# Performance work log

Measured on AMD Instinct MI355X. Metric: run time of the kernel, lower is better.

## Reference

```python
import jax, jax.numpy as jnp
import numpy as np

EPS = 1e-6
NUM_HEADS = 8


def layer_norm(x, g, b):
    m = jnp.mean(x, axis=-1, keepdims=True)
    v = jnp.mean(jnp.square(x - m), axis=-1, keepdims=True)
    return (x - m) * jax.lax.rsqrt(v + EPS) * g + b


def dwconv3x3(x, w, b):
    # x: [B, C, H, W], w: [C, 1, 3, 3] depthwise, b: [C]
    y = jax.lax.conv_general_dilated(
        x, w, window_strides=(1, 1), padding='SAME',
        feature_group_count=x.shape[1],
        dimension_numbers=('NCHW', 'OIHW', 'NCHW'))
    return y + b[None, :, None, None]


def setup_inputs() -> dict:
    key = jax.random.key(0)
    ks = jax.random.split(key, 16)
    B, H, W, C = 4, 128, 128, 256
    N = H * W
    hid = 3 * C  # mlp_ratio=3
    s = 0.02
    return {
        'x': jax.random.normal(ks[0], (B, N, C), jnp.float32),
        'H': H,
        'W': W,
        'ln1_g': jnp.ones((C,), jnp.float32),
        'ln1_b': jnp.zeros((C,), jnp.float32),
        'qkv_w': jax.random.normal(ks[1], (C, 3 * C), jnp.float32) * s,
        'qkv_b': jnp.zeros((3 * C,), jnp.float32),
        'crpe_w': jax.random.normal(ks[2], (C, 1, 3, 3), jnp.float32) * s,
        'crpe_b': jnp.zeros((C,), jnp.float32),
        'proj_w': jax.random.normal(ks[3], (C, C), jnp.float32) * s,
        'proj_b': jnp.zeros((C,), jnp.float32),
        'ln2_g': jnp.ones((C,), jnp.float32),
        'ln2_b': jnp.zeros((C,), jnp.float32),
        'fc1_w': jax.random.normal(ks[4], (C, hid), jnp.float32) * s,
        'fc1_b': jnp.zeros((hid,), jnp.float32),
        'dconv_w': jax.random.normal(ks[5], (hid, 1, 3, 3), jnp.float32) * s,
        'dconv_b': jnp.zeros((hid,), jnp.float32),
        'fc2_w': jax.random.normal(ks[6], (hid, C), jnp.float32) * s,
        'fc2_b': jnp.zeros((C,), jnp.float32),
    }


def reference(x, H, W, ln1_g, ln1_b, qkv_w, qkv_b, crpe_w, crpe_b,
              proj_w, proj_b, ln2_g, ln2_b, fc1_w, fc1_b,
              dconv_w, dconv_b, fc2_w, fc2_b):
    B, N, C = x.shape
    h = NUM_HEADS
    d = C // h
    scale = d ** -0.5

    # --- attention branch ---
    cur = layer_norm(x, ln1_g, ln1_b)
    qkv = (cur @ qkv_w + qkv_b).reshape(B, N, 3, h, d).transpose(2, 0, 3, 1, 4)
    q, k, v = qkv[0], qkv[1], qkv[2]          # each [B, h, N, d]
    k_sm = jax.nn.softmax(k, axis=2)          # softmax over tokens N
    kv = jnp.einsum('bhnk,bhnv->bhkv', k_sm, v)      # [B, h, d, d]
    factor = jnp.einsum('bhnk,bhkv->bhnv', q, kv)    # [B, h, N, d]
    # CRPE: q * depthwise_conv(v) on the HxW grid (head-major channel layout)
    v_img = v.transpose(0, 1, 3, 2).reshape(B, C, H, W)
    conv_v = dwconv3x3(v_img, crpe_w, crpe_b).reshape(B, h, d, N).transpose(0, 1, 3, 2)
    att = scale * factor + q * conv_v         # [B, h, N, d]
    att = att.transpose(0, 2, 1, 3).reshape(B, N, C)
    x = x + (att @ proj_w + proj_b)

    # --- conv-MLP branch ---
    cur = layer_norm(x, ln2_g, ln2_b)
    hdn = cur @ fc1_w + fc1_b                 # [B, N, 3C]
    hdn_img = hdn.transpose(0, 2, 1).reshape(B, hdn.shape[-1], H, W)
    dc = dwconv3x3(hdn_img, dconv_w, dconv_b).reshape(B, hdn.shape[-1], N).transpose(0, 2, 1)
    hdn = jax.nn.gelu(hdn + dc, approximate=False)
    return x + (hdn @ fc2_w + fc2_b)
```

## Files before the change

### kernel.cpp

```cpp
#include <hip/hip_runtime.h>
#include <math.h>

#define BB   4
#define HH   128
#define WW2  128
#define NN   (HH*WW2)
#define CC   256
#define NH   8
#define HID  768
#define EPSF 1e-6f
#define SCALE 0.17677669529663687f

typedef __attribute__((ext_vector_type(8))) short s8v;
typedef __attribute__((ext_vector_type(4))) float f4v;

__device__ __forceinline__ float bf2f(ushort h) {
    union { unsigned u; float f; } x; x.u = ((unsigned)h) << 16; return x.f;
}
__device__ __forceinline__ ushort f2bf(float f) {
    union { float f; unsigned u; } x; x.f = f;
    unsigned r = (x.u + 0x7FFFu + ((x.u >> 16) & 1u)) >> 16;
    return (ushort)r;
}

typedef __attribute__((address_space(1))) unsigned gu32;
typedef __attribute__((address_space(3))) unsigned lu32;
__device__ __forceinline__ void gl_lds16(const void* g, void* l) {
    __builtin_amdgcn_global_load_lds((gu32*)g, (lu32*)l, 16, 0, 0);
}

__global__ __launch_bounds__(256) void ln_bf16v(const float* __restrict__ in,
                                                const float* __restrict__ g,
                                                const float* __restrict__ bta,
                                                ushort* __restrict__ out) {
    int row  = blockIdx.x*4 + (threadIdx.x >> 6);
    int lane = threadIdx.x & 63;
    const float* p = in + (size_t)row*CC + lane*4;
    float4 v = *(const float4*)p;
    float s  = v.x + v.y + v.z + v.w;
    float s2 = v.x*v.x + v.y*v.y + v.z*v.z + v.w*v.w;
    #pragma unroll
    for (int off = 32; off >= 1; off >>= 1) {
        s  += __shfl_xor(s, off);
        s2 += __shfl_xor(s2, off);
    }
    float mean = s * (1.0f/CC);
    float var  = s2 * (1.0f/CC) - mean*mean;
    float r    = rsqrtf(var + EPSF);
    float4 gv = *(const float4*)&g[lane*4];
    float4 bv = *(const float4*)&bta[lane*4];
    ushort4 o;
    o.x = f2bf((v.x-mean)*r*gv.x + bv.x);
    o.y = f2bf((v.y-mean)*r*gv.y + bv.y);
    o.z = f2bf((v.z-mean)*r*gv.z + bv.z);
    o.w = f2bf((v.w-mean)*r*gv.w + bv.w);
    *(ushort4*)&out[(size_t)row*CC + lane*4] = o;
}

__global__ __launch_bounds__(256) void wtrans(const float* __restrict__ w,
                                              ushort* __restrict__ wt, int K, int N) {
    __shared__ float tile[32][33];
    int k0 = blockIdx.x*32, n0 = blockIdx.y*32;
    int c = threadIdx.x & 31, r8 = threadIdx.x >> 5;
    #pragma unroll
    for (int r = 0; r < 4; ++r) {
        int kk = r8 + r*8;
        tile[kk][c] = w[(size_t)(k0+kk)*N + n0 + c];
    }
    __syncthreads();
    #pragma unroll
    for (int r = 0; r < 4; ++r) {
        int nn = r8 + r*8;
        wt[(size_t)(n0+nn)*K + k0 + c] = f2bf(tile[c][nn]);
    }
}

__global__ __launch_bounds__(256) void wtrans_proj(const float* __restrict__ w,
                                                   ushort* __restrict__ Bcat) {
    __shared__ float tile[32][33];
    int k0 = blockIdx.x*32, n0 = blockIdx.y*32;
    int c = threadIdx.x & 31, r8 = threadIdx.x >> 5;
    #pragma unroll
    for (int r = 0; r < 4; ++r) {
        int kk = r8 + r*8;
        tile[kk][c] = w[(size_t)(k0+kk)*CC + n0 + c];
    }
    __syncthreads();
    #pragma unroll
    for (int r = 0; r < 4; ++r) {
        int nn = r8 + r*8;
        ushort val = f2bf(tile[c][nn]);
        #pragma unroll
        for (int b = 0; b < BB; ++b)
            Bcat[((size_t)(b*256 + n0+nn))*512 + 256 + k0 + c] = val;
    }
}

template<int KDIM, int MODE>
__global__ __launch_bounds__(256) void mfma_gemm(const ushort* __restrict__ A,
                                                 const ushort* __restrict__ Bt,
                                                 const float* __restrict__ bias,
                                                 const float* __restrict__ resid,
                                                 void* __restrict__ Cout,
                                                 ushort* __restrict__ kbuf,
                                                 ushort* __restrict__ vbuf,
                                                 int NDIM) {
    __shared__ ushort lsA[128*32];
    __shared__ ushort lsB[128*32];
    int tid  = threadIdx.x;
    int lane = tid & 63;
    int w    = tid >> 6;
    int wm   = w >> 1, wn = w & 1;
    size_t mBase = (size_t)blockIdx.y * 128;
    int    nBase = blockIdx.x * 128;
    int lrow = lane & 15, lq = lane >> 4;

    const ushort* gA = A  + (mBase + w*32 + (lane>>2))*(size_t)KDIM + (lane&3)*8;
    const ushort* gB = Bt + ((size_t)(nBase + w*32 + (lane>>2)))*(size_t)KDIM + (lane&3)*8;
    ushort* lA = lsA + w*1024;
    ushort* lB = lsB + w*1024;

    f4v acc[4][4] = {};

    for (int k0 = 0; k0 < KDIM; k0 += 32) {
        gl_lds16(gA + k0,           lA);
        gl_lds16(gA + k0 + 16*KDIM, lA + 512);
        gl_lds16(gB + k0,           lB);
        gl_lds16(gB + k0 + 16*KDIM, lB + 512);
        __syncthreads();
        s8v af[4], bf[4];
        #pragma unroll
        for (int i = 0; i < 4; ++i)
            af[i] = *(const s8v*)&lsA[(wm*64 + i*16 + lrow)*32 + lq*8];
        #pragma unroll
        for (int j = 0; j < 4; ++j)
            bf[j] = *(const s8v*)&lsB[(wn*64 + j*16 + lrow)*32 + lq*8];
        #pragma unroll
        for (int i = 0; i < 4; ++i)
            #pragma unroll
            for (int j = 0; j < 4; ++j)
                acc[i][j] = __builtin_amdgcn_mfma_f32_16x16x32_bf16(af[i], bf[j], acc[i][j], 0, 0, 0);
        __syncthreads();
    }

    int colBase = nBase + wn*64;
    #pragma unroll
    for (int j = 0; j < 4; ++j) {
        int col = colBase + j*16 + lrow;
        float bs = bias[col];
        #pragma unroll
        for (int i = 0; i < 4; ++i) {
            #pragma unroll
            for (int r = 0; r < 4; ++r) {
                size_t row = mBase + wm*64 + i*16 + lq*4 + r;
                float v = acc[i][j][r] + bs;
                if constexpr (MODE == 0) {
                    ((ushort*)Cout)[row*(size_t)NDIM + col] = f2bf(v);
                } else if constexpr (MODE == 1) {
                    size_t idx = row*(size_t)NDIM + col;
                    ((float*)Cout)[idx] = v + resid[idx];
                } else {
                    if (col < 256)      ((ushort*)Cout)[row*512 + col] = f2bf(v);
                    else if (col < 512) kbuf[row*256 + col - 256] = f2bf(v);
                    else                vbuf[row*256 + col - 512] = f2bf(v);
                }
            }
        }
    }
}

__global__ __launch_bounds__(256) void mfma_gemm_attn(const ushort* __restrict__ aq,
                                                      const ushort* __restrict__ Bcat,
                                                      const float* __restrict__ bias,
                                                      const float* __restrict__ resid,
                                                      float* __restrict__ Cout) {
    __shared__ ushort lsA[128*32];
    __shared__ ushort lsB[128*32];
    int tid  = threadIdx.x;
    int lane = tid & 63;
    int w    = tid >> 6;
    int wm   = w >> 1, wn = w & 1;
    int b = blockIdx.z;
    size_t mBase = (size_t)b*NN + (size_t)blockIdx.y * 128;
    int    nBase = blockIdx.x * 128;
    int lrow = lane & 15, lq = lane >> 4;

    const ushort* gA = aq + (mBase + w*32 + (lane>>2))*512 + (lane&3)*8;
    const ushort* gB = Bcat + ((size_t)(b*256 + nBase + w*32 + (lane>>2)))*512 + (lane&3)*8;
    ushort* lA = lsA + w*1024;
    ushort* lB = lsB + w*1024;

    f4v acc[4][4] = {};

    for (int k0 = 0; k0 < 512; k0 += 32) {
        gl_lds16(gA + k0,          lA);
        gl_lds16(gA + k0 + 16*512, lA + 512);
        gl_lds16(gB + k0,          lB);
        gl_lds16(gB + k0 + 16*512, lB + 512);
        __syncthreads();
        s8v af[4], bf[4];
        #pragma unroll
        for (int i = 0; i < 4; ++i)
            af[i] = *(const s8v*)&lsA[(wm*64 + i*16 + lrow)*32 + lq*8];
        #pragma unroll
        for (int j = 0; j < 4; ++j)
            bf[j] = *(const s8v*)&lsB[(wn*64 + j*16 + lrow)*32 + lq*8];
        #pragma unroll
        for (int i = 0; i < 4; ++i)
            #pragma unroll
            for (int j = 0; j < 4; ++j)
                acc[i][j] = __builtin_amdgcn_mfma_f32_16x16x32_bf16(af[i], bf[j], acc[i][j], 0, 0, 0);
        __syncthreads();
    }

    int colBase = nBase + wn*64;
    #pragma unroll
    for (int j = 0; j < 4; ++j) {
        int col = colBase + j*16 + lrow;
        float bs = bias[col];
        #pragma unroll
        for (int i = 0; i < 4; ++i) {
            #pragma unroll
            for (int r = 0; r < 4; ++r) {
                size_t row = mBase + wm*64 + i*16 + lq*4 + r;
                size_t idx = row*(size_t)CC + col;
                Cout[idx] = acc[i][j][r] + bs + resid[idx];
            }
        }
    }
}

__global__ void zero_kernel(float* __restrict__ p, int nElems) {
    int i = blockIdx.x*256 + threadIdx.x;
    if (i < nElems) p[i] = 0.f;
}

__global__ __launch_bounds__(256) void kv_accum(const ushort* __restrict__ kbuf,
                                                const ushort* __restrict__ vbuf,
                                                float* __restrict__ kv_raw,
                                                float* __restrict__ ksum) {
    int blk = blockIdx.x;
    int chunk = blk & 15;
    int bh = blk >> 4;
    int b = bh >> 3, hh = bh & 7;
    int tid = threadIdx.x;
    __shared__ float ke[32][36];
    __shared__ float vv[32][36];
    int tok = tid >> 3;
    int c4  = (tid & 7) * 4;
    int kd  = tid >> 3;
    int v0  = (tid & 7) * 4;
    float acc0=0.f, acc1=0.f, acc2=0.f, acc3=0.f, ks=0.f;
    for (int it = 0; it < 32; ++it) {
        int nb = chunk*1024 + it*32;
        size_t rowoff = ((size_t)b*NN + nb + tok)*256 + hh*32 + c4;
        ushort4 k4 = *(const ushort4*)&kbuf[rowoff];
        ushort4 v4 = *(const ushort4*)&vbuf[rowoff];
        float4 kf, vf;
        kf.x = expf(bf2f(k4.x)); kf.y = expf(bf2f(k4.y));
        kf.z = expf(bf2f(k4.z)); kf.w = expf(bf2f(k4.w));
        vf.x = bf2f(v4.x); vf.y = bf2f(v4.y); vf.z = bf2f(v4.z); vf.w = bf2f(v4.w);
        *(float4*)&ke[tok][c4] = kf;
        *(float4*)&vv[tok][c4] = vf;
        __syncthreads();
        #pragma unroll
        for (int tt = 0; tt < 32; ++tt) {
            float kval = ke[tt][kd];
            float4 vr = *(const float4*)&vv[tt][v0];
            ks   += kval;
            acc0 += kval*vr.x;
            acc1 += kval*vr.y;
            acc2 += kval*vr.z;
            acc3 += kval*vr.w;
        }
        __syncthreads();
    }
    float* dst = kv_raw + ((size_t)bh*32 + kd)*32 + v0;
    atomicAdd(dst+0, acc0); atomicAdd(dst+1, acc1);
    atomicAdd(dst+2, acc2); atomicAdd(dst+3, acc3);
    if (v0 == 0) atomicAdd(&ksum[bh*32 + kd], ks);
}

__global__ __launch_bounds__(256) void kv_fold(const float* __restrict__ kv_raw,
                                               const float* __restrict__ ksum,
                                               const float* __restrict__ proj_w,
                                               ushort* __restrict__ Bcat) {
    int bh = blockIdx.x;
    int b = bh >> 3, hh = bh & 7;
    int tid = threadIdx.x;
    __shared__ float kvn[32][33];
    __shared__ float pw[32][256];
    {
        int kd = tid >> 3, v4 = (tid & 7) * 4;
        float inv = 1.0f / ksum[bh*32 + kd];
        const float* src = kv_raw + ((size_t)bh*32 + kd)*32 + v4;
        kvn[kd][v4+0] = src[0]*inv; kvn[kd][v4+1] = src[1]*inv;
        kvn[kd][v4+2] = src[2]*inv; kvn[kd][v4+3] = src[3]*inv;
    }
    for (int vd = 0; vd < 32; ++vd)
        pw[vd][tid] = proj_w[(size_t)(hh*32 + vd)*CC + tid];
    __syncthreads();
    ushort* dst = Bcat + ((size_t)(b*256 + tid))*512 + hh*32;
    for (int kd = 0; kd < 32; ++kd) {
        float acc = 0.f;
        #pragma unroll
        for (int vd = 0; vd < 32; ++vd) acc += kvn[kd][vd] * pw[vd][tid];
        dst[kd] = f2bf(SCALE * acc);
    }
}

__global__ __launch_bounds__(256) void attn_gate(const ushort* __restrict__ vbuf,
                                                 const float* __restrict__ w,
                                                 const float* __restrict__ wb,
                                                 ushort* __restrict__ aq) {
    int xq = blockIdx.x, yq = blockIdx.y, b = blockIdx.z;
    int c = threadIdx.x;
    int y0 = yq*2;

    const float* wc = w + c*9;
    float w00=wc[0], w01=wc[1], w02=wc[2],
          w10=wc[3], w11=wc[4], w12=wc[5],
          w20=wc[6], w21=wc[7], w22=wc[8];
    float bw = wb[c];

    const ushort* vbase = vbuf + (size_t)b*NN*256 + c;
    auto ldv = [&](int yy, int xx) -> float {
        if ((unsigned)yy >= (unsigned)HH || (unsigned)xx >= (unsigned)WW2) return 0.f;
        return bf2f(vbase[((size_t)yy*WW2 + xx)*256]);
    };

    int x0 = xq*32;
    float rp[4], rc[4];
    #pragma unroll
    for (int r = 0; r < 4; ++r) {
        rp[r] = ldv(y0-1+r, x0-1);
        rc[r] = ldv(y0-1+r, x0);
    }

    #pragma unroll 4
    for (int i = 0; i < 32; ++i) {
        int x = x0 + i;
        float rn[4];
        #pragma unroll
        for (int r = 0; r < 4; ++r) rn[r] = ldv(y0-1+r, x+1);
        #pragma unroll
        for (int o = 0; o < 2; ++o) {
            float conv = bw + w00*rp[o] + w01*rc[o] + w02*rn[o]
                            + w10*rp[o+1] + w11*rc[o+1] + w12*rn[o+1]
                            + w20*rp[o+2] + w21*rc[o+2] + w22*rn[o+2];
            size_t bn = (size_t)b*NN + (size_t)(y0+o)*WW2 + x;
            float qc = bf2f(aq[bn*512 + c]);
            aq[bn*512 + 256 + c] = f2bf(qc*conv);
        }
        #pragma unroll
        for (int r = 0; r < 4; ++r) { rp[r] = rc[r]; rc[r] = rn[r]; }
    }
}

__global__ __launch_bounds__(384) void dconv_gelu_row2(const ushort* __restrict__ hdn,
                                                       const float* __restrict__ w,
                                                       const float* __restrict__ bias,
                                                       ushort* __restrict__ out) {
    int xq = blockIdx.x, yq = blockIdx.y, bz = blockIdx.z;
    int c = threadIdx.x * 2;
    int y0 = yq*2;

    float wA[9], wB[9];
    #pragma unroll
    for (int i = 0; i < 9; ++i) { wA[i] = w[c*9 + i]; wB[i] = w[(c+1)*9 + i]; }
    float bw0 = bias[c], bw1 = bias[c+1];

    const ushort* base = hdn + (size_t)bz*NN*HID + c;
    auto ld2 = [&](int yy, int xx) -> float2 {
        if ((unsigned)yy >= (unsigned)HH || (unsigned)xx >= (unsigned)WW2)
            return make_float2(0.f, 0.f);
        ushort2 u = *(const ushort2*)&base[((size_t)yy*WW2 + xx)*HID];
        return make_float2(bf2f(u.x), bf2f(u.y));
    };

    int x0 = xq*32;
    float2 rp[4], rc[4];
    #pragma unroll
    for (int r = 0; r < 4; ++r) {
        rp[r] = ld2(y0-1+r, x0-1);
        rc[r] = ld2(y0-1+r, x0);
    }

    #pragma unroll 4
    for (int i = 0; i < 32; ++i) {
        int x = x0 + i;
        float2 rn[4];
        #pragma unroll
        for (int r = 0; r < 4; ++r) rn[r] = ld2(y0-1+r, x+1);
        #pragma unroll
        for (int o = 0; o < 2; ++o) {
            float conv0 = bw0 + wA[0]*rp[o].x + wA[1]*rc[o].x + wA[2]*rn[o].x
                              + wA[3]*rp[o+1].x + wA[4]*rc[o+1].x + wA[5]*rn[o+1].x
                              + wA[6]*rp[o+2].x + wA[7]*rc[o+2].x + wA[8]*rn[o+2].x;
            float conv1 = bw1 + wB[0]*rp[o].y + wB[1]*rc[o].y + wB[2]*rn[o].y
                              + wB[3]*rp[o+1].y + wB[4]*rc[o+1].y + wB[5]*rn[o+1].y
                              + wB[6]*rp[o+2].y + wB[7]*rc[o+2].y + wB[8]*rn[o+2].y;
            float v0 = rc[o+1].x + conv0;
            float v1 = rc[o+1].y + conv1;
            ushort2 res;
            res.x = f2bf(0.5f*v0*(1.f + erff(v0*0.70710678118654752f)));
            res.y = f2bf(0.5f*v1*(1.f + erff(v1*0.70710678118654752f)));
            size_t n = (size_t)bz*NN + (size_t)(y0+o)*WW2 + x;
            *(ushort2*)&out[n*HID + c] = res;
        }
        #pragma unroll
        for (int r = 0; r < 4; ++r) { rp[r] = rc[r]; rc[r] = rn[r]; }
    }
}

extern "C" void kernel_launch(void* const* d_in, const int* in_sizes, int n_in,
                              void* d_out, int out_size, void* d_ws, size_t ws_size,
                              hipStream_t stream) {
    const float* x      = (const float*)d_in[0];
    const float* ln1_g  = (const float*)d_in[3];
    const float* ln1_b  = (const float*)d_in[4];
    const float* qkv_w  = (const float*)d_in[5];
    const float* qkv_b  = (const float*)d_in[6];
    const float* crpe_w = (const float*)d_in[7];
    const float* crpe_b = (const float*)d_in[8];
    const float* proj_w = (const float*)d_in[9];
    const float* proj_b = (const float*)d_in[10];
    const float* ln2_g  = (const float*)d_in[11];
    const float* ln2_b  = (const float*)d_in[12];
    const float* fc1_w  = (const float*)d_in[13];
    const float* fc1_b  = (const float*)d_in[14];
    const float* dconv_w= (const float*)d_in[15];
    const float* dconv_b= (const float*)d_in[16];
    const float* fc2_w  = (const float*)d_in[17];
    const float* fc2_b  = (const float*)d_in[18];
    float* outF = (float*)d_out;
    ushort* ws16 = (ushort*)d_ws;

    ushort* aq    = ws16;
    ushort* kbuf  = aq + 33554432;
    ushort* vbuf  = kbuf + 16777216;
    ushort* sbuf  = vbuf + 16777216;
    ushort* wqkvT = sbuf + 16777216;
    ushort* wfc1T = wqkvT + 196608;
    ushort* wfc2T = wfc1T + 196608;
    ushort* Bcat  = wfc2T + 196608;
    float*  kvraw = (float*)(Bcat + 524288);
    float*  ksumB = kvraw + 32768;
    ushort* hdn   = ws16;
    ushort* hdn2  = vbuf;

    const int ROWS = BB*NN;

    wtrans<<<dim3(8,24), 256, 0, stream>>>(qkv_w,  wqkvT, CC,  3*CC);
    wtrans<<<dim3(8,24), 256, 0, stream>>>(fc1_w,  wfc1T, CC,  HID);
    wtrans<<<dim3(24,8), 256, 0, stream>>>(fc2_w,  wfc2T, HID, CC);
    wtrans_proj<<<dim3(8,8), 256, 0, stream>>>(proj_w, Bcat);

    ln_bf16v<<<ROWS/4, 256, 0, stream>>>(x, ln1_g, ln1_b, sbuf);
    mfma_gemm<256, 2><<<dim3(6, 512), 256, 0, stream>>>(
        sbuf, wqkvT, qkv_b, nullptr, aq, kbuf, vbuf, 0);
    zero_kernel<<<132, 256, 0, stream>>>(kvraw, 32768 + 1024);
    kv_accum<<<BB*NH*16, 256, 0, stream>>>(kbuf, vbuf, kvraw, ksumB);
    kv_fold<<<32, 256, 0, stream>>>(kvraw, ksumB, proj_w, Bcat);
    attn_gate<<<dim3(4, 64, 4), 256, 0, stream>>>(vbuf, crpe_w, crpe_b, aq);
    mfma_gemm_attn<<<dim3(2, 128, 4), 256, 0, stream>>>(aq, Bcat, proj_b, x, outF);

    ln_bf16v<<<ROWS/4, 256, 0, stream>>>(outF, ln2_g, ln2_b, sbuf);
    mfma_gemm<256, 0><<<dim3(6, 512), 256, 0, stream>>>(
        sbuf, wfc1T, fc1_b, nullptr, hdn, nullptr, nullptr, 768);
    for (int p = 0; p < 2; ++p) {
        const ushort* hdn_p = hdn + (size_t)p*2*NN*HID;
        float* xo = outF + (size_t)p*2*NN*CC;
        dconv_gelu_row2<<<dim3(4, 64, 2), 384, 0, stream>>>(hdn_p, dconv_w, dconv_b, hdn2);
        mfma_gemm<768, 1><<<dim3(2, 256), 256, 0, stream>>>(
            hdn2, wfc2T, fc2_b, xo, xo, nullptr, nullptr, 256);
    }
}
```

Baseline: 651.5 us.

## Double-buffer LDS tiles in MFMA GEMMs and swizzle workgroup order

Both GEMM kernels now keep two LDS buffers, so the global-to-LDS loads for the next K step are issued before the MFMAs on the current step. This halves the barriers per iteration and hides load latency, at the cost of twice the LDS per workgroup, which may reduce occupancy. A modulo-8 remap of the workgroup index is also added, intended to improve L2 locality and XCD distribution. The swizzle assumes the tile count is divisible by 8.

```diff
diff --git a/kernel.cpp b/kernel.cpp
--- a/kernel.cpp
+++ b/kernel.cpp
@@ -105,42 +105,63 @@
                                                  ushort* __restrict__ kbuf,
                                                  ushort* __restrict__ vbuf,
                                                  int NDIM) {
-    __shared__ ushort lsA[128*32];
-    __shared__ ushort lsB[128*32];
+    __shared__ ushort lsA[2][128*32];
+    __shared__ ushort lsB[2][128*32];
     int tid  = threadIdx.x;
     int lane = tid & 63;
     int w    = tid >> 6;
     int wm   = w >> 1, wn = w & 1;
-    size_t mBase = (size_t)blockIdx.y * 128;
-    int    nBase = blockIdx.x * 128;
+
+    int nwg = gridDim.x * gridDim.y;
+    int lin = blockIdx.y * gridDim.x + blockIdx.x;
+    int swz = (lin & 7) * (nwg >> 3) + (lin >> 3);
+    int bx  = swz % gridDim.x;
+    int by  = swz / gridDim.x;
+
+    size_t mBase = (size_t)by * 128;
+    int    nBase = bx * 128;
     int lrow = lane & 15, lq = lane >> 4;
 
     const ushort* gA = A  + (mBase + w*32 + (lane>>2))*(size_t)KDIM + (lane&3)*8;
     const ushort* gB = Bt + ((size_t)(nBase + w*32 + (lane>>2)))*(size_t)KDIM + (lane&3)*8;
-    ushort* lA = lsA + w*1024;
-    ushort* lB = lsB + w*1024;
+    ushort* lA0 = lsA[0] + w*1024;  ushort* lA1 = lsA[1] + w*1024;
+    ushort* lB0 = lsB[0] + w*1024;  ushort* lB1 = lsB[1] + w*1024;
 
     f4v acc[4][4] = {};
 
-    for (int k0 = 0; k0 < KDIM; k0 += 32) {
-        gl_lds16(gA + k0,           lA);
-        gl_lds16(gA + k0 + 16*KDIM, lA + 512);
-        gl_lds16(gB + k0,           lB);
-        gl_lds16(gB + k0 + 16*KDIM, lB + 512);
-        __syncthreads();
-        s8v af[4], bf[4];
+    gl_lds16(gA,           lA0);
+    gl_lds16(gA + 16*KDIM, lA0 + 512);
+    gl_lds16(gB,           lB0);
+    gl_lds16(gB + 16*KDIM, lB0 + 512);
+    asm volatile("s_waitcnt vmcnt(0)" ::: "memory");
+    __builtin_amdgcn_s_barrier();
+
+    #pragma unroll
+    for (int kk = 0; kk < KDIM/32; ++kk) {
+        const int cur = kk & 1;
+        if (kk + 1 < KDIM/32) {
+            const int k1 = (kk+1)*32;
+            ushort* nA = cur ? lA0 : lA1;
+            ushort* nB = cur ? lB0 : lB1;
+            gl_lds16(gA + k1,           nA);
+            gl_lds16(gA + k1 + 16*KDIM, nA + 512);
+            gl_lds16(gB + k1,           nB);
+            gl_lds16(gB + k1 + 16*KDIM, nB + 512);
+        }
+        s8v af[4], bfr[4];
         #pragma unroll
         for (int i = 0; i < 4; ++i)
-            af[i] = *(const s8v*)&lsA[(wm*64 + i*16 + lrow)*32 + lq*8];
+            af[i] = *(const s8v*)&lsA[cur][(wm*64 + i*16 + lrow)*32 + lq*8];
         #pragma unroll
         for (int j = 0; j < 4; ++j)
-            bf[j] = *(const s8v*)&lsB[(wn*64 + j*16 + lrow)*32 + lq*8];
+            bfr[j] = *(const s8v*)&lsB[cur][(wn*64 + j*16 + lrow)*32 + lq*8];
         #pragma unroll
         for (int i = 0; i < 4; ++i)
             #pragma unroll
             for (int j = 0; j < 4; ++j)
-                acc[i][j] = __builtin_amdgcn_mfma_f32_16x16x32_bf16(af[i], bf[j], acc[i][j], 0, 0, 0);
-        __syncthreads();
+                acc[i][j] = __builtin_amdgcn_mfma_f32_16x16x32_bf16(af[i], bfr[j], acc[i][j], 0, 0, 0);
+        asm volatile("s_waitcnt vmcnt(0) lgkmcnt(0)" ::: "memory");
+        __builtin_amdgcn_s_barrier();
     }
 
     int colBase = nBase + wn*64;
@@ -174,43 +195,64 @@
                                                       const float* __restrict__ bias,
                                                       const float* __restrict__ resid,
                                                       float* __restrict__ Cout) {
-    __shared__ ushort lsA[128*32];
-    __shared__ ushort lsB[128*32];
+    __shared__ ushort lsA[2][128*32];
+    __shared__ ushort lsB[2][128*32];
     int tid  = threadIdx.x;
     int lane = tid & 63;
     int w    = tid >> 6;
     int wm   = w >> 1, wn = w & 1;
     int b = blockIdx.z;
-    size_t mBase = (size_t)b*NN + (size_t)blockIdx.y * 128;
-    int    nBase = blockIdx.x * 128;
+
+    int nwg = gridDim.x * gridDim.y;
+    int lin = blockIdx.y * gridDim.x + blockIdx.x;
+    int swz = (lin & 7) * (nwg >> 3) + (lin >> 3);
+    int bx  = swz % gridDim.x;
+    int by  = swz / gridDim.x;
+
+    size_t mBase = (size_t)b*NN + (size_t)by * 128;
+    int    nBase = bx * 128;
     int lrow = lane & 15, lq = lane >> 4;
 
     const ushort* gA = aq + (mBase + w*32 + (lane>>2))*512 + (lane&3)*8;
     const ushort* gB = Bcat + ((size_t)(b*256 + nBase + w*32 + (lane>>2)))*512 + (lane&3)*8;
-    ushort* lA = lsA + w*1024;
-    ushort* lB = lsB + w*1024;
+    ushort* lA0 = lsA[0] + w*1024;  ushort* lA1 = lsA[1] + w*1024;
+    ushort* lB0 = lsB[0] + w*1024;  ushort* lB1 = lsB[1] + w*1024;
 
     f4v acc[4][4] = {};
 
-    for (int k0 = 0; k0 < 512; k0 += 32) {
-        gl_lds16(gA + k0,          lA);
-        gl_lds16(gA + k0 + 16*512, lA + 512);
-        gl_lds16(gB + k0,          lB);
-        gl_lds16(gB + k0 + 16*512, lB + 512);
-        __syncthreads();
-        s8v af[4], bf[4];
+    gl_lds16(gA,          lA0);
+    gl_lds16(gA + 16*512, lA0 + 512);
+    gl_lds16(gB,          lB0);
+    gl_lds16(gB + 16*512, lB0 + 512);
+    asm volatile("s_waitcnt vmcnt(0)" ::: "memory");
+    __builtin_amdgcn_s_barrier();
+
+    #pragma unroll
+    for (int kk = 0; kk < 512/32; ++kk) {
+        const int cur = kk & 1;
+        if (kk + 1 < 512/32) {
+            const int k1 = (kk+1)*32;
+            ushort* nA = cur ? lA0 : lA1;
+            ushort* nB = cur ? lB0 : lB1;
+            gl_lds16(gA + k1,          nA);
+            gl_lds16(gA + k1 + 16*512, nA + 512);
+            gl_lds16(gB + k1,          nB);
+            gl_lds16(gB + k1 + 16*512, nB + 512);
+        }
+        s8v af[4], bfr[4];
         #pragma unroll
         for (int i = 0; i < 4; ++i)
-            af[i] = *(const s8v*)&lsA[(wm*64 + i*16 + lrow)*32 + lq*8];
+            af[i] = *(const s8v*)&lsA[cur][(wm*64 + i*16 + lrow)*32 + lq*8];
         #pragma unroll
         for (int j = 0; j < 4; ++j)
-            bf[j] = *(const s8v*)&lsB[(wn*64 + j*16 + lrow)*32 + lq*8];
+            bfr[j] = *(const s8v*)&lsB[cur][(wn*64 + j*16 + lrow)*32 + lq*8];
         #pragma unroll
         for (int i = 0; i < 4; ++i)
             #pragma unroll
             for (int j = 0; j < 4; ++j)
-                acc[i][j] = __builtin_amdgcn_mfma_f32_16x16x32_bf16(af[i], bf[j], acc[i][j], 0, 0, 0);
-        __syncthreads();
+                acc[i][j] = __builtin_amdgcn_mfma_f32_16x16x32_bf16(af[i], bfr[j], acc[i][j], 0, 0, 0);
+        asm volatile("s_waitcnt vmcnt(0) lgkmcnt(0)" ::: "memory");
+        __builtin_amdgcn_s_barrier();
     }
 
     int colBase = nBase + wn*64;
```

After: 662.1 us. Within noise of the previous version (+1.6%).
